# Optimization experiments

Hardware: AMD Instinct MI355X
Metric: run time of the kernel (lower is better)

Reference implementation:

```python
import jax, jax.numpy as jnp
import numpy as np

N, E = 100000, 800000
D_IN, D_HID, D_OUT = 128, 128, 40


def _lin_params(key, d_out, d_in, bias):
    k1, k2 = jax.random.split(key)
    bound = 1.0 / np.sqrt(d_in)
    W = jax.random.uniform(k1, (d_out, d_in), jnp.float32, -bound, bound)
    if bias:
        b = jax.random.uniform(k2, (d_out,), jnp.float32, -bound, bound)
        return W, b
    return W


def setup_inputs() -> dict:
    key = jax.random.key(0)
    ks = jax.random.split(key, 8)
    x = jax.random.normal(ks[0], (N, D_IN), jnp.float32)
    edge_index = jax.random.randint(ks[1], (2, E), 0, N, jnp.int64)
    Wl0, b0 = _lin_params(ks[2], D_HID, D_IN, True)
    Wr0 = _lin_params(ks[3], D_HID, D_IN, False)
    Wl1, b1 = _lin_params(ks[4], D_HID, D_HID, True)
    Wr1 = _lin_params(ks[5], D_HID, D_HID, False)
    Wl2, b2 = _lin_params(ks[6], D_OUT, D_HID, True)
    Wr2 = _lin_params(ks[7], D_OUT, D_HID, False)
    return {"x": x, "edge_index": edge_index,
            "Wl0": Wl0, "Wr0": Wr0, "b0": b0,
            "Wl1": Wl1, "Wr1": Wr1, "b1": b1,
            "Wl2": Wl2, "Wr2": Wr2, "b2": b2}


def _sage_conv(x, src, dst, Wl, Wr, b):
    # mean aggregation of neighbor messages (src -> dst), PyG SAGEConv semantics
    msg = x[src]                                               # [E, d]
    agg = jax.ops.segment_sum(msg, dst, num_segments=N)        # [N, d]
    deg = jax.ops.segment_sum(jnp.ones((src.shape[0],), x.dtype), dst,
                              num_segments=N)                  # [N]
    agg = agg / jnp.maximum(deg, 1.0)[:, None]
    # out = lin_l(agg) + lin_r(x); lin_l has bias, lin_r does not
    return agg @ Wl.T + x @ Wr.T + b


def reference(x, edge_index, Wl0, Wr0, b0, Wl1, Wr1, b1, Wl2, Wr2, b2):
    src, dst = edge_index[0], edge_index[1]
    h = jax.nn.relu(_sage_conv(x, src, dst, Wl0, Wr0, b0))   # dropout = identity in eval
    h = jax.nn.relu(_sage_conv(h, src, dst, Wl1, Wr1, b1))
    h = _sage_conv(h, src, dst, Wl2, Wr2, b2)
    return jax.nn.log_softmax(h, axis=1)
```

## Files before the change

kernel.cpp:

```cpp
#include <hip/hip_runtime.h>
#include <hip/hip_bf16.h>
#include <math.h>

#define D 128
typedef unsigned int uint;
typedef unsigned short ushort;

using bf16x8 = __attribute__((ext_vector_type(8))) short;
using f32x4  = __attribute__((ext_vector_type(4))) float;
using f32x2  = __attribute__((ext_vector_type(2))) float;

static __device__ __forceinline__ ushort f2b(float f) {
    __hip_bfloat16 h = __float2bfloat16(f);
    return __builtin_bit_cast(ushort, h);
}
static __device__ __forceinline__ float blo(uint u) {
    uint v = u << 16;
    return __builtin_bit_cast(float, v);
}
static __device__ __forceinline__ float bhi(uint u) {
    uint v = u & 0xFFFF0000u;
    return __builtin_bit_cast(float, v);
}

#define NBLK_A 1024
#define MAXB   128
#define WTOT   (2*128*256 + 80*128)

__global__ __launch_bounds__(256) void k_bcount(
    const int* __restrict__ dst, int* __restrict__ cnt, int E, int nbuck,
    const float* __restrict__ x, ushort* __restrict__ Abuf, int n4,
    const float* __restrict__ Wl0, const float* __restrict__ Wr0,
    const float* __restrict__ Wl1, const float* __restrict__ Wr1,
    const float* __restrict__ Wl2, const float* __restrict__ Wr2,
    ushort* __restrict__ Wtg0, ushort* __restrict__ Wtg1,
    ushort* __restrict__ W2tg)
{
    __shared__ int h[MAXB];
    int tid = threadIdx.x, b = blockIdx.x;
    for (int k = tid; k < nbuck; k += 256) h[k] = 0;
    __syncthreads();
    int chunk = (E + NBLK_A - 1) / NBLK_A;
    int beg = b * chunk, end = min(beg + chunk, E);
    for (int e = beg + tid; e < end; e += 256)
        atomicAdd(&h[dst[e] >> 10], 1);
    __syncthreads();
    for (int k = tid; k < nbuck; k += 256) cnt[k * NBLK_A + b] = h[k];

    for (int i = b * 256 + tid; i < n4; i += NBLK_A * 256) {
        float4 v = *(const float4*)(x + (size_t)i * 4);
        int node = i >> 5, coff = (i & 31) * 4;
        ushort4 o;
        o.x = f2b(v.x); o.y = f2b(v.y); o.z = f2b(v.z); o.w = f2b(v.w);
        *(ushort4*)(Abuf + (size_t)node * 256 + 128 + coff) = o;
    }
    for (int i = b * 256 + tid; i < WTOT; i += NBLK_A * 256) {
        if (i < 2 * 128 * 256) {
            int which = i >> 15;
            int o = i & 32767;
            int j = o >> 8, kk = o & 255;
            const float* Wl = which ? Wl1 : Wl0;
            const float* Wr = which ? Wr1 : Wr0;
            float v = (kk < 128) ? Wl[j * 128 + kk] : Wr[j * 128 + (kk - 128)];
            (which ? Wtg1 : Wtg0)[o] = f2b(v);
        } else {
            int o = i - 2 * 128 * 256;
            int j = o >> 7, kk = o & 127;
            float v = (j < 40) ? Wl2[j * 128 + kk] : Wr2[(j - 40) * 128 + kk];
            W2tg[o] = f2b(v);
        }
    }
}

__global__ __launch_bounds__(256) void k_scanA(int* __restrict__ a,
                                               int* __restrict__ bsum, int n) {
    __shared__ int s[256];
    int tid = threadIdx.x;
    int i = blockIdx.x * 256 + tid;
    int v = (i < n) ? a[i] : 0;
    s[tid] = v;
    __syncthreads();
#pragma unroll
    for (int o = 1; o < 256; o <<= 1) {
        int t = (tid >= o) ? s[tid - o] : 0;
        __syncthreads();
        s[tid] += t;
        __syncthreads();
    }
    if (i < n) a[i] = s[tid] - v;
    if (tid == 255) bsum[blockIdx.x] = s[255];
}

__global__ void k_scan2(int* __restrict__ bsum, int nb) {
    __shared__ int s[512];
    __shared__ int carry_s;
    int tid = threadIdx.x;
    if (tid == 0) carry_s = 0;
    __syncthreads();
    for (int base = 0; base < nb; base += 512) {
        int i = base + tid;
        int v = (i < nb) ? bsum[i] : 0;
        s[tid] = v;
        __syncthreads();
#pragma unroll
        for (int o = 1; o < 512; o <<= 1) {
            int t = (tid >= o) ? s[tid - o] : 0;
            __syncthreads();
            s[tid] += t;
            __syncthreads();
        }
        int carry = carry_s;
        if (i < nb) bsum[i] = s[tid] - v + carry;
        int total = s[511];
        __syncthreads();
        if (tid == 0) carry_s = carry + total;
        __syncthreads();
    }
}

__global__ __launch_bounds__(256) void k_scanB(int* __restrict__ a,
                                               const int* __restrict__ bsum,
                                               int* __restrict__ bb,
                                               int n, int nbuck, int E) {
    int i = blockIdx.x * 256 + threadIdx.x;
    if (i < n) {
        int v = a[i] + bsum[blockIdx.x];
        a[i] = v;
        if ((i & (NBLK_A - 1)) == 0) bb[i / NBLK_A] = v;
    }
    if (i == 0) bb[nbuck] = E;
}

__global__ __launch_bounds__(256) void k_bplace(
    const int* __restrict__ src, const int* __restrict__ dst,
    const int* __restrict__ cnt, uint2* __restrict__ ebuf, int E, int nbuck)
{
    __shared__ int cur[MAXB];
    int tid = threadIdx.x, b = blockIdx.x;
    for (int k = tid; k < nbuck; k += 256) cur[k] = cnt[k * NBLK_A + b];
    __syncthreads();
    int chunk = (E + NBLK_A - 1) / NBLK_A;
    int beg = b * chunk, end = min(beg + chunk, E);
    for (int e = beg + tid; e < end; e += 256) {
        int d = dst[e];
        int r = atomicAdd(&cur[d >> 10], 1);
        ebuf[r] = make_uint2((uint)src[e], (uint)d);
    }
}

__global__ __launch_bounds__(1024) void k_bfine(
    const uint2* __restrict__ ebuf, const int* __restrict__ bb,
    int* __restrict__ rowptr, int* __restrict__ col, int nN, int nbuck, int E)
{
    __shared__ int cnt2[1024];
    __shared__ int sc[1024];
    int k = blockIdx.x, tid = threadIdx.x;
    int e0 = bb[k], e1 = bb[k + 1];
    cnt2[tid] = 0;
    __syncthreads();
    for (int e = e0 + tid; e < e1; e += 1024)
        atomicAdd(&cnt2[ebuf[e].y & 1023], 1);
    __syncthreads();
    int v = cnt2[tid];
    sc[tid] = v;
    __syncthreads();
#pragma unroll
    for (int o = 1; o < 1024; o <<= 1) {
        int t = (tid >= o) ? sc[tid - o] : 0;
        __syncthreads();
        sc[tid] += t;
        __syncthreads();
    }
    int excl = sc[tid] - v;
    int node = k * 1024 + tid;
    if (node < nN) rowptr[node] = e0 + excl;
    if (k == nbuck - 1 && tid == 0) rowptr[nN] = E;
    cnt2[tid] = e0 + excl;
    __syncthreads();
    for (int e = e0 + tid; e < e1; e += 1024) {
        uint2 sd = ebuf[e];
        int r = atomicAdd(&cnt2[sd.y & 1023], 1);
        col[r] = (int)sd.x;
    }
}

__global__ __launch_bounds__(256) void k_gather128(
    const ushort* __restrict__ feat, ushort* __restrict__ agg,
    const int* __restrict__ rowptr, const int* __restrict__ col, int nN)
{
    int tid = threadIdx.x;
    int lane = tid & 63;
    int h = lane >> 5;
    int node = blockIdx.x * 8 + ((tid >> 6) << 1) + h;
    if (node >= nN) return;
    int g = (lane >> 4) & 1;
    int r = lane & 15;
    int beg = rowptr[node], end = rowptr[node + 1];
    const char* fb = (const char*)feat;
    const uint rb = (uint)(r << 4);
    float a[8];
#pragma unroll
    for (int i = 0; i < 8; ++i) a[i] = 0.f;

    int j = beg + g;
    for (; j + 2 < end; j += 4) {
        int s0 = col[j], s1 = col[j + 2];
        uint4 v0 = *(const uint4*)(fb + (((uint)s0 << 9) + rb));
        uint4 v1 = *(const uint4*)(fb + (((uint)s1 << 9) + rb));
        const uint* p0 = (const uint*)&v0;
        const uint* p1 = (const uint*)&v1;
#pragma unroll
        for (int i = 0; i < 4; ++i) {
            a[2 * i]     += blo(p0[i]) + blo(p1[i]);
            a[2 * i + 1] += bhi(p0[i]) + bhi(p1[i]);
        }
    }
    if (j < end) {
        int s0 = col[j];
        uint4 v0 = *(const uint4*)(fb + (((uint)s0 << 9) + rb));
        const uint* p0 = (const uint*)&v0;
#pragma unroll
        for (int i = 0; i < 4; ++i) {
            a[2 * i]     += blo(p0[i]);
            a[2 * i + 1] += bhi(p0[i]);
        }
    }
#pragma unroll
    for (int i = 0; i < 8; ++i)
        a[i] += __shfl_xor(a[i], 16);
    if (g == 0) {
        float inv = 1.0f / (float)max(end - beg, 1);
        uint4 o;
        uint* po = (uint*)&o;
#pragma unroll
        for (int i = 0; i < 4; ++i)
            po[i] = (uint)f2b(a[2 * i] * inv) | ((uint)f2b(a[2 * i + 1] * inv) << 16);
        *(uint4*)(agg + (size_t)node * 256 + r * 8) = o;
    }
}

template<int OUTJ, int KDIM, int SW, int MODE>
__global__ __launch_bounds__(256) void k_gemm_mfma(
    const ushort* __restrict__ A, int astride,
    const ushort* __restrict__ Wt, const float* __restrict__ bias,
    ushort* __restrict__ out, int ostride, ushort* __restrict__ out2, int nN)
{
    constexpr int NT = OUTJ / 16;
    constexpr int KSTEPS = KDIM / 32;
    __shared__ __align__(16) ushort Ws[OUTJ * SW];

    const int tid = threadIdx.x;
    constexpr int CHUNKS = OUTJ * KDIM / 8;
#pragma unroll
    for (int c = tid; c < CHUNKS; c += 256) {
        int row = c / (KDIM / 8);
        int ko  = (c % (KDIM / 8)) * 8;
        *(uint4*)(Ws + row * SW + ko) = *(const uint4*)(Wt + row * KDIM + ko);
    }
    __syncthreads();

    const int l = tid & 63, wv = tid >> 6;
    const int q = l >> 4, r = l & 15;
    const long long m0 = (long long)blockIdx.x * 128 + wv * 32;
    const int mA = (int)min(m0 + r, (long long)(nN - 1));
    const int mB = (int)min(m0 + 16 + r, (long long)(nN - 1));
    const ushort* pa = A + (size_t)mA * astride + q * 8;
    const ushort* pb = A + (size_t)mB * astride + q * 8;

    f32x4 acc[2][NT];
#pragma unroll
    for (int mt = 0; mt < 2; ++mt)
#pragma unroll
        for (int nt = 0; nt < NT; ++nt)
            acc[mt][nt] = (f32x4){0.f, 0.f, 0.f, 0.f};

    bf16x8 a0 = *(const bf16x8*)pa;
    bf16x8 a1 = *(const bf16x8*)pb;
#pragma unroll
    for (int ks = 0; ks < KSTEPS; ++ks) {
        bf16x8 a0n = a0, a1n = a1;
        if (ks + 1 < KSTEPS) {
            a0n = *(const bf16x8*)(pa + (ks + 1) * 32);
            a1n = *(const bf16x8*)(pb + (ks + 1) * 32);
        }
#pragma unroll
        for (int nt = 0; nt < NT; ++nt) {
            bf16x8 b = *(const bf16x8*)(Ws + (nt * 16 + r) * SW + ks * 32 + q * 8);
            acc[0][nt] = __builtin_amdgcn_mfma_f32_16x16x32_bf16(a0, b, acc[0][nt], 0, 0, 0);
            acc[1][nt] = __builtin_amdgcn_mfma_f32_16x16x32_bf16(a1, b, acc[1][nt], 0, 0, 0);
        }
        a0 = a0n; a1 = a1n;
    }

#pragma unroll
    for (int mt = 0; mt < 2; ++mt) {
#pragma unroll
        for (int i = 0; i < 4; ++i) {
            long long m = m0 + mt * 16 + q * 4 + i;
            if (m >= nN) continue;
#pragma unroll
            for (int nt = 0; nt < NT; ++nt) {
                int cc = nt * 16 + r;
                float v = acc[mt][nt][i];
                if (MODE == 0) {
                    v += bias[cc];
                    v = fmaxf(v, 0.f);
                    out[(size_t)m * ostride + cc] = f2b(v);
                } else {
                    if (cc < 40) out[(size_t)m * 40 + cc] = f2b(v);
                    else { v += bias[cc - 40]; out2[(size_t)m * 40 + (cc - 40)] = f2b(v); }
                }
            }
        }
    }
}

__global__ __launch_bounds__(256) void k_gather40_lsm(
    const ushort* __restrict__ P, const ushort* __restrict__ R,
    const int* __restrict__ rowptr, const int* __restrict__ col,
    float* __restrict__ out, int nN)
{
    int tid = threadIdx.x;
    int lane = tid & 63;
    int h = lane >> 4;
    int node = blockIdx.x * 16 + ((tid >> 6) << 2) + h;
    if (node >= nN) return;
    int g = (lane >> 3) & 1;
    int r = lane & 7;
    int beg = rowptr[node], end = rowptr[node + 1];
    const char* pbase = (const char*)P;
    const uint rb = (uint)(r << 4);
    f32x2 a2[4];
#pragma unroll
    for (int i = 0; i < 4; ++i) a2[i] = (f32x2){0.f, 0.f};

    int j = beg + g;
    for (; j + 2 < end; j += 4) {
        int s0 = col[j], s1 = col[j + 2];
        uint4 v0 = *(const uint4*)(pbase + ((((uint)s0 * 5u) << 4) + rb));
        uint4 v1 = *(const uint4*)(pbase + ((((uint)s1 * 5u) << 4) + rb));
        const uint* p0 = (const uint*)&v0;
        const uint* p1 = (const uint*)&v1;
#pragma unroll
        for (int i = 0; i < 4; ++i)
            a2[i] += (f32x2){blo(p0[i]) + blo(p1[i]), bhi(p0[i]) + bhi(p1[i])};
    }
    if (j < end) {
        int s0 = col[j];
        uint4 v0 = *(const uint4*)(pbase + ((((uint)s0 * 5u) << 4) + rb));
        const uint* p0 = (const uint*)&v0;
#pragma unroll
        for (int i = 0; i < 4; ++i)
            a2[i] += (f32x2){blo(p0[i]), bhi(p0[i])};
    }
    float a[8];
#pragma unroll
    for (int i = 0; i < 4; ++i) { a[2 * i] = a2[i].x; a[2 * i + 1] = a2[i].y; }
#pragma unroll
    for (int i = 0; i < 8; ++i)
        a[i] += __shfl_xor(a[i], 8);
    float inv = 1.0f / (float)max(end - beg, 1);
    uint4 rv = *(const uint4*)(R + (size_t)node * 40 + r * 8);
    const uint* pr = (const uint*)&rv;
    float vv[8];
    float mx = -INFINITY;
#pragma unroll
    for (int i = 0; i < 8; ++i) {
        float rc = (i & 1) ? bhi(pr[i >> 1]) : blo(pr[i >> 1]);
        int c = r * 8 + i;
        vv[i] = (c < 40) ? (a[i] * inv + rc) : -INFINITY;
        mx = fmaxf(mx, vv[i]);
    }
    mx = fmaxf(mx, __shfl_xor(mx, 1));
    mx = fmaxf(mx, __shfl_xor(mx, 2));
    mx = fmaxf(mx, __shfl_xor(mx, 4));
    float s = 0.f;
#pragma unroll
    for (int i = 0; i < 8; ++i) {
        int c = r * 8 + i;
        if (c < 40) s += __expf(vv[i] - mx);
    }
    s += __shfl_xor(s, 1);
    s += __shfl_xor(s, 2);
    s += __shfl_xor(s, 4);
    float lse = mx + __logf(s);
    if (g == 0 && r < 5) {
        float4 o0 = make_float4(vv[0] - lse, vv[1] - lse, vv[2] - lse, vv[3] - lse);
        float4 o1 = make_float4(vv[4] - lse, vv[5] - lse, vv[6] - lse, vv[7] - lse);
        *(float4*)(out + (size_t)node * 40 + r * 8)     = o0;
        *(float4*)(out + (size_t)node * 40 + r * 8 + 4) = o1;
    }
}

extern "C" void kernel_launch(void* const* d_in, const int* in_sizes, int n_in,
                              void* d_out, int out_size, void* d_ws, size_t ws_size,
                              hipStream_t stream) {
    const float* x   = (const float*)d_in[0];
    const int*   ei  = (const int*)d_in[1];
    const float* Wl0 = (const float*)d_in[2];
    const float* Wr0 = (const float*)d_in[3];
    const float* b0  = (const float*)d_in[4];
    const float* Wl1 = (const float*)d_in[5];
    const float* Wr1 = (const float*)d_in[6];
    const float* b1  = (const float*)d_in[7];
    const float* Wl2 = (const float*)d_in[8];
    const float* Wr2 = (const float*)d_in[9];
    const float* b2  = (const float*)d_in[10];
    const int nN = in_sizes[0] / D;
    const int E  = in_sizes[1] / 2;
    const int* src = ei;
    const int* dst = ei + E;

    char* w = (char*)d_ws;
    auto alloc = [&](size_t bytes) { char* p = w; w += (bytes + 255) & ~(size_t)255; return p; };
    const int nbuck = (nN + 1023) >> 10;
    const int ncnt  = nbuck * NBLK_A;
    int*    cnt    = (int*)   alloc((size_t)ncnt * 4);
    int*    bsum   = (int*)   alloc((size_t)((ncnt + 255) / 256) * 4);
    int*    bb     = (int*)   alloc((size_t)(nbuck + 1) * 4);
    int*    rowptr = (int*)   alloc((size_t)(nN + 1) * 4);
    int*    col    = (int*)   alloc((size_t)E * 4);
    ushort* AbufA  = (ushort*)alloc((size_t)nN * 256 * 2);
    ushort* AbufB  = (ushort*)alloc((size_t)nN * 256 * 2);
    ushort* Wtg0   = (ushort*)alloc((size_t)128 * 256 * 2);
    ushort* Wtg1   = (ushort*)alloc((size_t)128 * 256 * 2);
    ushort* W2tg   = (ushort*)alloc((size_t)80 * 128 * 2);
    uint2*  ebuf   = (uint2*)AbufB;
    ushort* Pbuf   = AbufB;
    ushort* Rbuf   = AbufB + (size_t)nN * 40;
    float*  logits = (float*)d_out;

    const int GATH_BLKS = (nN + 7) / 8;
    const int G40_BLKS  = (nN + 15) / 16;
    const int GEMM_BLKS = (nN + 127) / 128;
    const int n4        = nN * 32;
    const int NBSC      = (ncnt + 255) / 256;

    k_bcount<<<NBLK_A, 256, 0, stream>>>(dst, cnt, E, nbuck, x, AbufA, n4,
                                         Wl0, Wr0, Wl1, Wr1, Wl2, Wr2,
                                         Wtg0, Wtg1, W2tg);
    k_scanA <<<NBSC, 256, 0, stream>>>(cnt, bsum, ncnt);
    k_scan2 <<<1, 512, 0, stream>>>(bsum, NBSC);
    k_scanB <<<NBSC, 256, 0, stream>>>(cnt, bsum, bb, ncnt, nbuck, E);
    k_bplace<<<NBLK_A, 256, 0, stream>>>(src, dst, cnt, ebuf, E, nbuck);
    k_bfine <<<nbuck, 1024, 0, stream>>>(ebuf, bb, rowptr, col, nN, nbuck, E);

    k_gather128<<<GATH_BLKS, 256, 0, stream>>>(AbufA + 128, AbufA, rowptr, col, nN);
    k_gemm_mfma<128, 256, 264, 0><<<GEMM_BLKS, 256, 0, stream>>>(
        AbufA, 256, Wtg0, b0, AbufB + 128, 256, nullptr, nN);

    k_gather128<<<GATH_BLKS, 256, 0, stream>>>(AbufB + 128, AbufB, rowptr, col, nN);
    k_gemm_mfma<128, 256, 264, 0><<<GEMM_BLKS, 256, 0, stream>>>(
        AbufB, 256, Wtg1, b1, AbufA + 128, 256, nullptr, nN);

    k_gemm_mfma<80, 128, 136, 1><<<GEMM_BLKS, 256, 0, stream>>>(
        AbufA + 128, 256, W2tg, b2, Pbuf, 40, Rbuf, nN);
    k_gather40_lsm<<<G40_BLKS, 256, 0, stream>>>(Pbuf, Rbuf, rowptr, col, logits, nN);
}
```

Baseline: 297.0 us.

## Fuse neighbor gather with MFMA GEMM and fold scan fixup into consumers

Replaces the separate mean-aggregation gather and MFMA GEMM for the two hidden layers with one kernel. It aggregates 128 nodes into shared memory and then runs the MFMA matmul against the concatenated [agg | self] features, with bias and ReLU applied in the epilogue. This removes the global write and re-read of the aggregated buffer and one launch per layer. It also drops the k_scanB pass: bplace adds the block sum itself and scan2 writes the bucket boundaries. In exchange, weights are now read directly from global memory instead of staged in LDS, and the gather phase runs with lower occupancy because of the large shared buffer.

```diff
diff --git a/kernel.cpp b/kernel.cpp
--- a/kernel.cpp
+++ b/kernel.cpp
@@ -91,7 +91,8 @@
     if (tid == 255) bsum[blockIdx.x] = s[255];
 }
 
-__global__ void k_scan2(int* __restrict__ bsum, int nb) {
+__global__ void k_scan2(int* __restrict__ bsum, int nb,
+                        int* __restrict__ bb, int nbuck, int E) {
     __shared__ int s[512];
     __shared__ int carry_s;
     int tid = threadIdx.x;
@@ -116,28 +117,21 @@
         if (tid == 0) carry_s = carry + total;
         __syncthreads();
     }
-}
-
-__global__ __launch_bounds__(256) void k_scanB(int* __restrict__ a,
-                                               const int* __restrict__ bsum,
-                                               int* __restrict__ bb,
-                                               int n, int nbuck, int E) {
-    int i = blockIdx.x * 256 + threadIdx.x;
-    if (i < n) {
-        int v = a[i] + bsum[blockIdx.x];
-        a[i] = v;
-        if ((i & (NBLK_A - 1)) == 0) bb[i / NBLK_A] = v;
-    }
-    if (i == 0) bb[nbuck] = E;
+    for (int k = tid; k < nbuck; k += 512) bb[k] = bsum[k * (NBLK_A >> 8)];
+    if (tid == 0) bb[nbuck] = E;
 }
 
 __global__ __launch_bounds__(256) void k_bplace(
     const int* __restrict__ src, const int* __restrict__ dst,
-    const int* __restrict__ cnt, uint2* __restrict__ ebuf, int E, int nbuck)
+    const int* __restrict__ cnt, const int* __restrict__ bsum,
+    uint2* __restrict__ ebuf, int E, int nbuck)
 {
     __shared__ int cur[MAXB];
     int tid = threadIdx.x, b = blockIdx.x;
-    for (int k = tid; k < nbuck; k += 256) cur[k] = cnt[k * NBLK_A + b];
+    for (int k = tid; k < nbuck; k += 256) {
+        int idx = k * NBLK_A + b;
+        cur[k] = cnt[idx] + bsum[idx >> 8];
+    }
     __syncthreads();
     int chunk = (E + NBLK_A - 1) / NBLK_A;
     int beg = b * chunk, end = min(beg + chunk, E);
@@ -184,58 +178,117 @@
     }
 }
 
-__global__ __launch_bounds__(256) void k_gather128(
-    const ushort* __restrict__ feat, ushort* __restrict__ agg,
+__global__ __launch_bounds__(256) void k_fused128(
+    const ushort* __restrict__ featc,
+    const ushort* __restrict__ Wt,
+    const float* __restrict__ bias,
+    ushort* __restrict__ out,
     const int* __restrict__ rowptr, const int* __restrict__ col, int nN)
 {
-    int tid = threadIdx.x;
-    int lane = tid & 63;
-    int h = lane >> 5;
-    int node = blockIdx.x * 8 + ((tid >> 6) << 1) + h;
-    if (node >= nN) return;
-    int g = (lane >> 4) & 1;
-    int r = lane & 15;
-    int beg = rowptr[node], end = rowptr[node + 1];
-    const char* fb = (const char*)feat;
-    const uint rb = (uint)(r << 4);
-    float a[8];
-#pragma unroll
-    for (int i = 0; i < 8; ++i) a[i] = 0.f;
-
-    int j = beg + g;
-    for (; j + 2 < end; j += 4) {
-        int s0 = col[j], s1 = col[j + 2];
-        uint4 v0 = *(const uint4*)(fb + (((uint)s0 << 9) + rb));
-        uint4 v1 = *(const uint4*)(fb + (((uint)s1 << 9) + rb));
-        const uint* p0 = (const uint*)&v0;
-        const uint* p1 = (const uint*)&v1;
+    __shared__ __align__(16) ushort agg[128 * 136];
+    const int tid = threadIdx.x;
+    const int lane = tid & 63, wv = tid >> 6;
+    const int m0 = blockIdx.x * 128;
+
+    {
+        int h = lane >> 5;
+        int g = (lane >> 4) & 1;
+        int r = lane & 15;
+        const char* fb = (const char*)featc;
+        const uint rb = (uint)(r << 4);
+        for (int p = 0; p < 16; ++p) {
+            int nl = p * 8 + (wv << 1) + h;
+            int node = m0 + nl;
+            float a[8];
+#pragma unroll
+            for (int i = 0; i < 8; ++i) a[i] = 0.f;
+            float inv = 0.f;
+            if (node < nN) {
+                int beg = rowptr[node], end = rowptr[node + 1];
+                int j = beg + g;
+                for (; j + 2 < end; j += 4) {
+                    int s0 = col[j], s1 = col[j + 2];
+                    uint4 v0 = *(const uint4*)(fb + (((uint)s0 << 9) + rb));
+                    uint4 v1 = *(const uint4*)(fb + (((uint)s1 << 9) + rb));
+                    const uint* p0 = (const uint*)&v0;
+                    const uint* p1 = (const uint*)&v1;
+#pragma unroll
+                    for (int i = 0; i < 4; ++i) {
+                        a[2 * i]     += blo(p0[i]) + blo(p1[i]);
+                        a[2 * i + 1] += bhi(p0[i]) + bhi(p1[i]);
+                    }
+                }
+                if (j < end) {
+                    int s0 = col[j];
+                    uint4 v0 = *(const uint4*)(fb + (((uint)s0 << 9) + rb));
+                    const uint* p0 = (const uint*)&v0;
+#pragma unroll
+                    for (int i = 0; i < 4; ++i) {
+                        a[2 * i]     += blo(p0[i]);
+                        a[2 * i + 1] += bhi(p0[i]);
+                    }
+                }
+#pragma unroll
+                for (int i = 0; i < 8; ++i)
+                    a[i] += __shfl_xor(a[i], 16);
+                inv = 1.0f / (float)max(end - beg, 1);
+            }
+            if (g == 0) {
+                uint4 o;
+                uint* po = (uint*)&o;
+#pragma unroll
+                for (int i = 0; i < 4; ++i)
+                    po[i] = (uint)f2b(a[2 * i] * inv) | ((uint)f2b(a[2 * i + 1] * inv) << 16);
+                *(uint4*)(agg + nl * 136 + r * 8) = o;
+            }
+        }
+    }
+    __syncthreads();
+
+    const int q = lane >> 4, r = lane & 15;
+    const int lA = wv * 32 + r, lB = wv * 32 + 16 + r;
+    const int mA = min(m0 + lA, nN - 1);
+    const int mB = min(m0 + lB, nN - 1);
+
+    f32x4 acc[2][8];
+#pragma unroll
+    for (int mt = 0; mt < 2; ++mt)
+#pragma unroll
+        for (int nt = 0; nt < 8; ++nt)
+            acc[mt][nt] = (f32x4){0.f, 0.f, 0.f, 0.f};
+
+#pragma unroll
+    for (int ks = 0; ks < 8; ++ks) {
+        bf16x8 a0, a1;
+        if (ks < 4) {
+            a0 = *(const bf16x8*)(agg + lA * 136 + ks * 32 + q * 8);
+            a1 = *(const bf16x8*)(agg + lB * 136 + ks * 32 + q * 8);
+        } else {
+            a0 = *(const bf16x8*)(featc + (size_t)mA * 256 + (ks - 4) * 32 + q * 8);
+            a1 = *(const bf16x8*)(featc + (size_t)mB * 256 + (ks - 4) * 32 + q * 8);
+        }
+#pragma unroll
+        for (int nt = 0; nt < 8; ++nt) {
+            bf16x8 b = *(const bf16x8*)(Wt + (nt * 16 + r) * 256 + ks * 32 + q * 8);
+            acc[0][nt] = __builtin_amdgcn_mfma_f32_16x16x32_bf16(a0, b, acc[0][nt], 0, 0, 0);
+            acc[1][nt] = __builtin_amdgcn_mfma_f32_16x16x32_bf16(a1, b, acc[1][nt], 0, 0, 0);
+        }
+    }
+
+#pragma unroll
+    for (int mt = 0; mt < 2; ++mt) {
 #pragma unroll
         for (int i = 0; i < 4; ++i) {
-            a[2 * i]     += blo(p0[i]) + blo(p1[i]);
-            a[2 * i + 1] += bhi(p0[i]) + bhi(p1[i]);
-        }
-    }
-    if (j < end) {
-        int s0 = col[j];
-        uint4 v0 = *(const uint4*)(fb + (((uint)s0 << 9) + rb));
-        const uint* p0 = (const uint*)&v0;
-#pragma unroll
-        for (int i = 0; i < 4; ++i) {
-            a[2 * i]     += blo(p0[i]);
-            a[2 * i + 1] += bhi(p0[i]);
-        }
-    }
-#pragma unroll
-    for (int i = 0; i < 8; ++i)
-        a[i] += __shfl_xor(a[i], 16);
-    if (g == 0) {
-        float inv = 1.0f / (float)max(end - beg, 1);
-        uint4 o;
-        uint* po = (uint*)&o;
-#pragma unroll
-        for (int i = 0; i < 4; ++i)
-            po[i] = (uint)f2b(a[2 * i] * inv) | ((uint)f2b(a[2 * i + 1] * inv) << 16);
-        *(uint4*)(agg + (size_t)node * 256 + r * 8) = o;
+            int m = m0 + wv * 32 + mt * 16 + q * 4 + i;
+            if (m >= nN) continue;
+#pragma unroll
+            for (int nt = 0; nt < 8; ++nt) {
+                int cc = nt * 16 + r;
+                float v = acc[mt][nt][i] + bias[cc];
+                v = fmaxf(v, 0.f);
+                out[(size_t)m * 256 + cc] = f2b(v);
+            }
+        }
     }
 }
 
@@ -430,7 +483,6 @@
     ushort* Rbuf   = AbufB + (size_t)nN * 40;
     float*  logits = (float*)d_out;
 
-    const int GATH_BLKS = (nN + 7) / 8;
     const int G40_BLKS  = (nN + 15) / 16;
     const int GEMM_BLKS = (nN + 127) / 128;
     const int n4        = nN * 32;
@@ -440,18 +492,15 @@
                                          Wl0, Wr0, Wl1, Wr1, Wl2, Wr2,
                                          Wtg0, Wtg1, W2tg);
     k_scanA <<<NBSC, 256, 0, stream>>>(cnt, bsum, ncnt);
-    k_scan2 <<<1, 512, 0, stream>>>(bsum, NBSC);
-    k_scanB <<<NBSC, 256, 0, stream>>>(cnt, bsum, bb, ncnt, nbuck, E);
-    k_bplace<<<NBLK_A, 256, 0, stream>>>(src, dst, cnt, ebuf, E, nbuck);
+    k_scan2 <<<1, 512, 0, stream>>>(bsum, NBSC, bb, nbuck, E);
+    k_bplace<<<NBLK_A, 256, 0, stream>>>(src, dst, cnt, bsum, ebuf, E, nbuck);
     k_bfine <<<nbuck, 1024, 0, stream>>>(ebuf, bb, rowptr, col, nN, nbuck, E);
 
-    k_gather128<<<GATH_BLKS, 256, 0, stream>>>(AbufA + 128, AbufA, rowptr, col, nN);
-    k_gemm_mfma<128, 256, 264, 0><<<GEMM_BLKS, 256, 0, stream>>>(
-        AbufA, 256, Wtg0, b0, AbufB + 128, 256, nullptr, nN);
-
-    k_gather128<<<GATH_BLKS, 256, 0, stream>>>(AbufB + 128, AbufB, rowptr, col, nN);
-    k_gemm_mfma<128, 256, 264, 0><<<GEMM_BLKS, 256, 0, stream>>>(
-        AbufB, 256, Wtg1, b1, AbufA + 128, 256, nullptr, nN);
+    k_fused128<<<GEMM_BLKS, 256, 0, stream>>>(
+        AbufA + 128, Wtg0, b0, AbufB + 128, rowptr, col, nN);
+
+    k_fused128<<<GEMM_BLKS, 256, 0, stream>>>(
+        AbufB + 128, Wtg1, b1, AbufA + 128, rowptr, col, nN);
 
     k_gemm_mfma<80, 128, 136, 1><<<GEMM_BLKS, 256, 0, stream>>>(
         AbufA + 128, 256, W2tg, b2, Pbuf, 40, Rbuf, nN);
```

Measured after the change: 418.8 us. 1.41x slower.
